# Optimization experiments

Measured on AMD Instinct MI355X. Metric: run time of the kernel, lower is better.

The kernel has to match this reference:

```python
import jax, jax.numpy as jnp
import numpy as np

J = 24
PARENTS = [-1, 0, 0, 0, 1, 2, 3, 4, 5, 6, 7, 8, 9, 9, 9, 12, 13, 14, 16, 17, 18, 19, 20, 21]


def _rodrigues(rvec):
    # rvec: [M,3] axis-angle -> [M,3,3] rotation matrices (Rodrigues formula)
    angle = jnp.linalg.norm(rvec, axis=-1, keepdims=True) + 1e-8  # [M,1]
    axis = rvec / angle
    s = jnp.sin(angle)[..., None]  # [M,1,1]
    c = jnp.cos(angle)[..., None]
    kx, ky, kz = axis[:, 0], axis[:, 1], axis[:, 2]
    zo = jnp.zeros_like(kx)
    K = jnp.stack([zo, -kz, ky, kz, zo, -kx, -ky, kx, zo], axis=-1).reshape(-1, 3, 3)
    eye = jnp.eye(3, dtype=rvec.dtype)
    return eye + s * K + (1.0 - c) * (K @ K)


def _get_tfs(poses, rest_joints, cano_inv=None):
    # poses: [B,J,3] -> relative transforms [B,J,4,4]
    B = poses.shape[0]
    R = _rodrigues(poses.reshape(-1, 3)).reshape(B, J, 3, 3)
    parents = np.asarray(PARENTS)
    rel_j = rest_joints.at[1:].add(-rest_joints[parents[1:]])  # [J,3]
    top = jnp.concatenate([R, jnp.broadcast_to(rel_j[None, :, :, None], (B, J, 3, 1))], axis=-1)
    bot = jnp.broadcast_to(jnp.array([0.0, 0.0, 0.0, 1.0], poses.dtype), (B, J, 1, 4))
    T = jnp.concatenate([top, bot], axis=-2)  # [B,J,4,4]
    chain = [T[:, 0]]
    for i in range(1, J):
        chain.append(chain[parents[i]] @ T[:, i])
    transforms = jnp.stack(chain, axis=1)  # [B,J,4,4]
    # subtract transforms @ [j;0] from the translation column
    tj = jnp.einsum('bjrc,jc->bjr', transforms[..., :3], rest_joints)  # [B,J,4]
    rel = jnp.concatenate([transforms[..., :3], (transforms[..., 3] - tj)[..., None]], axis=-1)
    if cano_inv is not None:
        rel = jnp.einsum('bnij,njk->bnik', rel, cano_inv)
    return rel


def _grid_sample_3d(grid, coords):
    # grid: [C,D,H,W]; coords: [P,3] normalized (x,y,z), align_corners=False, border padding
    C, D, H, W = grid.shape
    sizes = jnp.array([W, H, D], dtype=coords.dtype)
    c = ((coords + 1.0) * sizes - 1.0) * 0.5
    c = jnp.clip(c, 0.0, sizes - 1.0)
    c0f = jnp.floor(c)
    frac = c - c0f  # [P,3]
    c0 = c0f.astype(jnp.int32)
    cmax = (sizes - 1.0).astype(jnp.int32)
    c1 = jnp.minimum(c0 + 1, cmax)
    out = jnp.zeros((C, coords.shape[0]), dtype=grid.dtype)
    for dx in (0, 1):
        for dy in (0, 1):
            for dz in (0, 1):
                ix = c1[:, 0] if dx else c0[:, 0]
                iy = c1[:, 1] if dy else c0[:, 1]
                iz = c1[:, 2] if dz else c0[:, 2]
                wx = frac[:, 0] if dx else 1.0 - frac[:, 0]
                wy = frac[:, 1] if dy else 1.0 - frac[:, 1]
                wz = frac[:, 2] if dz else 1.0 - frac[:, 2]
                out = out + grid[:, iz, iy, ix] * (wx * wy * wz)[None, :]
    return out.T  # [P,C]


def _query_weights(verts, weight_grid, lhand_grid, rhand_grid,
                   bbox_extend, bbox_center, lhand_extend, lhand_center,
                   rhand_extend, rhand_center):
    B, N, _ = verts.shape
    p = ((verts - bbox_center[None, None]) / bbox_extend * 2.0).reshape(B * N, 3)
    w = _grid_sample_3d(weight_grid, p)  # [P,J]
    pl = p * lhand_extend + lhand_center[None]
    lmask = jnp.all((pl >= -1.0) & (pl <= 1.0), axis=-1)
    w = jnp.where(lmask[:, None], _grid_sample_3d(lhand_grid, pl), w)
    pr = p * rhand_extend + rhand_center[None]
    rmask = jnp.all((pr >= -1.0) & (pr <= 1.0), axis=-1)
    w = jnp.where(rmask[:, None], _grid_sample_3d(rhand_grid, pr), w)
    return w.reshape(B, N, J)


def setup_inputs() -> dict:
    key = jax.random.key(0)
    ks = jax.random.split(key, 8)
    B, N, R = 4, 65536, 128
    verts = jax.random.uniform(ks[0], (B, N, 3), jnp.float32, -0.9, 0.9)
    poses = jax.random.normal(ks[1], (B, J, 3), jnp.float32) * 0.2
    cano_pose = jax.random.normal(ks[2], (1, J, 3), jnp.float32) * 0.05
    rest_joints = jax.random.normal(ks[3], (J, 3), jnp.float32) * 0.3
    weight_grid = jax.random.uniform(ks[4], (J, R, R, R), jnp.float32)
    lhand_grid = jax.random.uniform(ks[5], (J, R, R, R), jnp.float32)
    rhand_grid = jax.random.uniform(ks[6], (J, R, R, R), jnp.float32)
    return dict(
        verts=verts, poses=poses, cano_pose=cano_pose, rest_joints=rest_joints,
        weight_grid=weight_grid, lhand_grid=lhand_grid, rhand_grid=rhand_grid,
        bbox_extend=jnp.float32(2.0), bbox_center=jnp.zeros((3,), jnp.float32),
        lhand_extend=jnp.float32(6.0), lhand_center=jnp.array([3.0, 1.2, 0.1], jnp.float32),
        rhand_extend=jnp.float32(6.0), rhand_center=jnp.array([-3.0, 1.2, 0.1], jnp.float32),
    )


def reference(verts, poses, cano_pose, rest_joints, weight_grid, lhand_grid, rhand_grid,
              bbox_extend, bbox_center, lhand_extend, lhand_center, rhand_extend, rhand_center):
    B, N = verts.shape[:2]
    cano_tfs = _get_tfs(cano_pose, rest_joints, None)        # [1,J,4,4]
    cano_inv = jnp.linalg.inv(cano_tfs[0])                   # [J,4,4]
    rel = _get_tfs(poses, rest_joints, cano_inv)             # [B,J,4,4]
    weights = _query_weights(verts, weight_grid, lhand_grid, rhand_grid,
                             bbox_extend, bbox_center, lhand_extend, lhand_center,
                             rhand_extend, rhand_center)     # [B,N,J]
    wt = jnp.matmul(weights, rel.reshape(B, J, 16)).reshape(B, N, 4, 4)
    posed = jnp.einsum('bnij,bnj->bni', wt[..., :3, :3], verts) + wt[..., :3, 3]
    return posed
```

## Files before the change

kernel.cpp:

```cpp
#include <hip/hip_runtime.h>
#include <math.h>

#define J 24
#define RES 128
#define DHW (RES*RES*RES)
#define NBINS 16384

__device__ __constant__ int PARENTS[J] = {-1,0,0,0,1,2,3,4,5,6,7,8,9,9,9,12,13,14,16,17,18,19,20,21};

__device__ inline void compose34(const float* a, const float* b, float* r) {
    for (int i = 0; i < 3; ++i) {
        float a0 = a[i*4+0], a1 = a[i*4+1], a2 = a[i*4+2], a3 = a[i*4+3];
        r[i*4+0] = a0*b[0] + a1*b[4] + a2*b[8];
        r[i*4+1] = a0*b[1] + a1*b[5] + a2*b[9];
        r[i*4+2] = a0*b[2] + a1*b[6] + a2*b[10];
        r[i*4+3] = a0*b[3] + a1*b[7] + a2*b[11] + a3;
    }
}

__global__ void tf_kernel(const float* __restrict__ poses,
                          const float* __restrict__ cano_pose,
                          const float* __restrict__ rest_joints,
                          float* __restrict__ rel_out) {
    __shared__ float M[5][J][12];
    __shared__ float relj[J][3];
    __shared__ float cinv[J][12];
    const int t = threadIdx.x;

    if (t < J) {
        int p = PARENTS[t];
        for (int k = 0; k < 3; ++k) {
            float v = rest_joints[t*3+k];
            if (p >= 0) v -= rest_joints[p*3+k];
            relj[t][k] = v;
        }
    }
    __syncthreads();

    for (int task = t; task < 5*J; task += blockDim.x) {
        int s = task / J, j = task % J;
        const float* rv = (s == 0) ? (cano_pose + j*3) : (poses + ((s-1)*J + j)*3);
        float rx = rv[0], ry = rv[1], rz = rv[2];
        float ang = sqrtf(rx*rx + ry*ry + rz*rz) + 1e-8f;
        float ax = rx/ang, ay = ry/ang, az = rz/ang;
        float s_ = sinf(ang), c_ = cosf(ang), ic = 1.0f - c_;
        float* m = M[s][j];
        m[0]  = 1.0f - ic*(ay*ay + az*az);
        m[1]  = -s_*az + ic*ax*ay;
        m[2]  =  s_*ay + ic*ax*az;
        m[3]  = relj[j][0];
        m[4]  =  s_*az + ic*ax*ay;
        m[5]  = 1.0f - ic*(ax*ax + az*az);
        m[6]  = -s_*ax + ic*ay*az;
        m[7]  = relj[j][1];
        m[8]  = -s_*ay + ic*ax*az;
        m[9]  =  s_*ax + ic*ay*az;
        m[10] = 1.0f - ic*(ax*ax + ay*ay);
        m[11] = relj[j][2];
    }
    __syncthreads();

    if (t < 5) {
        for (int i = 1; i < J; ++i) {
            int p = PARENTS[i];
            float r[12];
            compose34(M[t][p], M[t][i], r);
            for (int k = 0; k < 12; ++k) M[t][i][k] = r[k];
        }
    }
    __syncthreads();

    for (int task = t; task < 5*J; task += blockDim.x) {
        int s = task / J, j = task % J;
        float* m = M[s][j];
        float rjx = rest_joints[j*3], rjy = rest_joints[j*3+1], rjz = rest_joints[j*3+2];
        m[3]  -= m[0]*rjx + m[1]*rjy + m[2]*rjz;
        m[7]  -= m[4]*rjx + m[5]*rjy + m[6]*rjz;
        m[11] -= m[8]*rjx + m[9]*rjy + m[10]*rjz;
    }
    __syncthreads();

    if (t < J) {
        const float* m = M[0][t];
        float* ci = cinv[t];
        ci[0] = m[0]; ci[1] = m[4]; ci[2]  = m[8];
        ci[4] = m[1]; ci[5] = m[5]; ci[6]  = m[9];
        ci[8] = m[2]; ci[9] = m[6]; ci[10] = m[10];
        ci[3]  = -(ci[0]*m[3] + ci[1]*m[7] + ci[2]*m[11]);
        ci[7]  = -(ci[4]*m[3] + ci[5]*m[7] + ci[6]*m[11]);
        ci[11] = -(ci[8]*m[3] + ci[9]*m[7] + ci[10]*m[11]);
    }
    __syncthreads();

    for (int task = t; task < 4*J; task += blockDim.x) {
        int b = task / J, j = task % J;
        float r[12];
        compose34(M[b+1][j], cinv[j], r);
        for (int k = 0; k < 12; ++k) rel_out[(b*J + j)*12 + k] = r[k];
    }
}

__global__ void zero_kernel(unsigned int* __restrict__ p, int n) {
    int i = blockIdx.x * blockDim.x + threadIdx.x;
    if (i < n) p[i] = 0;
}

__device__ inline void main_grid_coords(float vx, float vy, float vz,
                                        float bcx, float bcy, float bcz, float be,
                                        float& px, float& py, float& pz,
                                        int& x0, int& y0, int& z0,
                                        float& tx, float& ty, float& tz) {
    px = (vx - bcx) / be * 2.0f;
    py = (vy - bcy) / be * 2.0f;
    pz = (vz - bcz) / be * 2.0f;
    const float S = (float)RES;
    float fx = ((px + 1.0f) * S - 1.0f) * 0.5f;
    float fy = ((py + 1.0f) * S - 1.0f) * 0.5f;
    float fz = ((pz + 1.0f) * S - 1.0f) * 0.5f;
    fx = fminf(fmaxf(fx, 0.0f), S - 1.0f);
    fy = fminf(fmaxf(fy, 0.0f), S - 1.0f);
    fz = fminf(fmaxf(fz, 0.0f), S - 1.0f);
    float x0f = floorf(fx), y0f = floorf(fy), z0f = floorf(fz);
    tx = fx - x0f; ty = fy - y0f; tz = fz - z0f;
    x0 = (int)x0f; y0 = (int)y0f; z0 = (int)z0f;
}

__global__ __launch_bounds__(256) void key_kernel(
    const float* __restrict__ verts,
    const float* __restrict__ bbox_extend, const float* __restrict__ bbox_center,
    unsigned int* __restrict__ keys, unsigned int* __restrict__ hist, int total) {
    int i = blockIdx.x * blockDim.x + threadIdx.x;
    if (i >= total) return;
    float vx = verts[(size_t)i*3+0], vy = verts[(size_t)i*3+1], vz = verts[(size_t)i*3+2];
    float px, py, pz, tx, ty, tz;
    int x0, y0, z0;
    main_grid_coords(vx, vy, vz, bbox_center[0], bbox_center[1], bbox_center[2],
                     bbox_extend[0], px, py, pz, x0, y0, z0, tx, ty, tz);
    unsigned int key = ((unsigned)z0 << 7) | (unsigned)y0;
    keys[i] = key;
    atomicAdd(&hist[key], 1u);
}

__global__ __launch_bounds__(1024) void scan_kernel(
    const unsigned int* __restrict__ hist, unsigned int* __restrict__ cursor) {
    __shared__ unsigned int partial[1024];
    const int t = threadIdx.x;
    const int CHUNK = NBINS / 1024;
    unsigned int local[CHUNK];
    unsigned int s = 0;
    #pragma unroll
    for (int k = 0; k < CHUNK; ++k) { local[k] = s; s += hist[t*CHUNK + k]; }
    partial[t] = s;
    __syncthreads();
    for (int off = 1; off < 1024; off <<= 1) {
        unsigned int v = (t >= off) ? partial[t - off] : 0u;
        __syncthreads();
        partial[t] += v;
        __syncthreads();
    }
    unsigned int excl = partial[t] - s;
    #pragma unroll
    for (int k = 0; k < CHUNK; ++k) cursor[t*CHUNK + k] = excl + local[k];
}

__global__ __launch_bounds__(256) void scatter_kernel(
    const unsigned int* __restrict__ keys, unsigned int* __restrict__ cursor,
    unsigned int* __restrict__ order, int total) {
    int i = blockIdx.x * blockDim.x + threadIdx.x;
    if (i >= total) return;
    unsigned int key = keys[i];
    unsigned int pos = atomicAdd(&cursor[key], 1u);
    order[pos] = (unsigned int)i;
}

__device__ inline void sample_grid_f32(const float* __restrict__ g,
                                       float cx, float cy, float cz, float* w) {
    const float S = (float)RES;
    float fx = ((cx + 1.0f) * S - 1.0f) * 0.5f;
    float fy = ((cy + 1.0f) * S - 1.0f) * 0.5f;
    float fz = ((cz + 1.0f) * S - 1.0f) * 0.5f;
    fx = fminf(fmaxf(fx, 0.0f), S - 1.0f);
    fy = fminf(fmaxf(fy, 0.0f), S - 1.0f);
    fz = fminf(fmaxf(fz, 0.0f), S - 1.0f);
    float x0f = floorf(fx), y0f = floorf(fy), z0f = floorf(fz);
    float tx = fx - x0f, ty = fy - y0f, tz = fz - z0f;
    int x0 = (int)x0f, y0 = (int)y0f, z0 = (int)z0f;
    int x1 = x0 < RES-1 ? x0+1 : RES-1;
    int y1 = y0 < RES-1 ? y0+1 : RES-1;
    int z1 = z0 < RES-1 ? z0+1 : RES-1;
    int b00 = (z0*RES + y0)*RES;
    int b01 = (z0*RES + y1)*RES;
    int b10 = (z1*RES + y0)*RES;
    int b11 = (z1*RES + y1)*RES;
    float wx0 = 1.0f - tx, wx1 = tx;
    float wy0 = 1.0f - ty, wy1 = ty;
    float wz0 = 1.0f - tz, wz1 = tz;
    float w000 = wz0*wy0*wx0, w001 = wz0*wy0*wx1;
    float w010 = wz0*wy1*wx0, w011 = wz0*wy1*wx1;
    float w100 = wz1*wy0*wx0, w101 = wz1*wy0*wx1;
    float w110 = wz1*wy1*wx0, w111 = wz1*wy1*wx1;
    #pragma unroll
    for (int c = 0; c < J; ++c) {
        const float* gc = g + (size_t)c * DHW;
        w[c] = gc[b00+x0]*w000 + gc[b00+x1]*w001
             + gc[b01+x0]*w010 + gc[b01+x1]*w011
             + gc[b10+x0]*w100 + gc[b10+x1]*w101
             + gc[b11+x0]*w110 + gc[b11+x1]*w111;
    }
}

__global__ __launch_bounds__(256) void skin_sorted(
    const float* __restrict__ verts,
    const float* __restrict__ wgrid,
    const float* __restrict__ lgrid,
    const float* __restrict__ rgrid,
    const float* __restrict__ rel,
    const unsigned int* __restrict__ order,
    const float* __restrict__ bbox_extend, const float* __restrict__ bbox_center,
    const float* __restrict__ lhand_extend, const float* __restrict__ lhand_center,
    const float* __restrict__ rhand_extend, const float* __restrict__ rhand_center,
    float* __restrict__ out, int N, int total) {
    __shared__ float srel[4*J*12];
    for (int i = threadIdx.x; i < 4*J*12; i += blockDim.x)
        srel[i] = rel[i];
    __syncthreads();

    int sid = blockIdx.x * blockDim.x + threadIdx.x;
    if (sid >= total) return;
    int pid = (int)order[sid];
    int b = pid / N;

    float vx = verts[(size_t)pid*3 + 0];
    float vy = verts[(size_t)pid*3 + 1];
    float vz = verts[(size_t)pid*3 + 2];

    float px, py, pz, tx, ty, tz;
    int x0, y0, z0;
    main_grid_coords(vx, vy, vz, bbox_center[0], bbox_center[1], bbox_center[2],
                     bbox_extend[0], px, py, pz, x0, y0, z0, tx, ty, tz);
    int x1 = x0 < RES-1 ? x0+1 : RES-1;
    int y1 = y0 < RES-1 ? y0+1 : RES-1;
    int z1 = z0 < RES-1 ? z0+1 : RES-1;
    int b00 = (z0*RES + y0)*RES;
    int b01 = (z0*RES + y1)*RES;
    int b10 = (z1*RES + y0)*RES;
    int b11 = (z1*RES + y1)*RES;
    float wx0 = 1.0f - tx, wx1 = tx;
    float wy0 = 1.0f - ty, wy1 = ty;
    float wz0 = 1.0f - tz, wz1 = tz;
    float w000 = wz0*wy0*wx0, w001 = wz0*wy0*wx1;
    float w010 = wz0*wy1*wx0, w011 = wz0*wy1*wx1;
    float w100 = wz1*wy0*wx0, w101 = wz1*wy0*wx1;
    float w110 = wz1*wy1*wx0, w111 = wz1*wy1*wx1;

    float w[J];
    #pragma unroll
    for (int c = 0; c < J; ++c) {
        const float* gc = wgrid + (size_t)c * DHW;
        w[c] = gc[b00+x0]*w000 + gc[b00+x1]*w001
             + gc[b01+x0]*w010 + gc[b01+x1]*w011
             + gc[b10+x0]*w100 + gc[b10+x1]*w101
             + gc[b11+x0]*w110 + gc[b11+x1]*w111;
    }

    float le = lhand_extend[0];
    float plx = px*le + lhand_center[0];
    float ply = py*le + lhand_center[1];
    float plz = pz*le + lhand_center[2];
    if (plx >= -1.0f && plx <= 1.0f && ply >= -1.0f && ply <= 1.0f &&
        plz >= -1.0f && plz <= 1.0f) {
        sample_grid_f32(lgrid, plx, ply, plz, w);
    }
    float re = rhand_extend[0];
    float prx = px*re + rhand_center[0];
    float pry = py*re + rhand_center[1];
    float prz = pz*re + rhand_center[2];
    if (prx >= -1.0f && prx <= 1.0f && pry >= -1.0f && pry <= 1.0f &&
        prz >= -1.0f && prz <= 1.0f) {
        sample_grid_f32(rgrid, prx, pry, prz, w);
    }

    const float* rb = &srel[b*J*12];
    float m[12];
    #pragma unroll
    for (int k = 0; k < 12; ++k) m[k] = 0.0f;
    #pragma unroll
    for (int j = 0; j < J; ++j) {
        float wj = w[j];
        const float* rj = &rb[j*12];
        #pragma unroll
        for (int k = 0; k < 12; ++k) m[k] += wj * rj[k];
    }

    out[(size_t)pid*3 + 0] = m[0]*vx + m[1]*vy + m[2]*vz  + m[3];
    out[(size_t)pid*3 + 1] = m[4]*vx + m[5]*vy + m[6]*vz  + m[7];
    out[(size_t)pid*3 + 2] = m[8]*vx + m[9]*vy + m[10]*vz + m[11];
}

extern "C" void kernel_launch(void* const* d_in, const int* in_sizes, int n_in,
                              void* d_out, int out_size, void* d_ws, size_t ws_size,
                              hipStream_t stream) {
    const float* verts       = (const float*)d_in[0];
    const float* poses       = (const float*)d_in[1];
    const float* cano_pose   = (const float*)d_in[2];
    const float* rest_joints = (const float*)d_in[3];
    const float* wgrid       = (const float*)d_in[4];
    const float* lgrid       = (const float*)d_in[5];
    const float* rgrid       = (const float*)d_in[6];
    const float* bbox_extend = (const float*)d_in[7];
    const float* bbox_center = (const float*)d_in[8];
    const float* lhand_extend= (const float*)d_in[9];
    const float* lhand_center= (const float*)d_in[10];
    const float* rhand_extend= (const float*)d_in[11];
    const float* rhand_center= (const float*)d_in[12];

    float* out = (float*)d_out;

    const int B = 4;
    const int total = in_sizes[0] / 3;
    const int N = total / B;

    char* ws = (char*)d_ws;
    float*        rel    = (float*)(ws);
    unsigned int* hist   = (unsigned int*)(ws + 8192);
    unsigned int* cursor = (unsigned int*)(ws + 8192 + 65536);
    unsigned int* keys   = (unsigned int*)(ws + 8192 + 2*65536);
    unsigned int* order  = (unsigned int*)(ws + 8192 + 2*65536 + (size_t)total*4);

    const int block = 256;
    const int pgrid = (total + block - 1) / block;

    tf_kernel<<<1, 128, 0, stream>>>(poses, cano_pose, rest_joints, rel);
    zero_kernel<<<(NBINS + block - 1) / block, block, 0, stream>>>(hist, NBINS);
    key_kernel<<<pgrid, block, 0, stream>>>(verts, bbox_extend, bbox_center,
                                            keys, hist, total);
    scan_kernel<<<1, 1024, 0, stream>>>(hist, cursor);
    scatter_kernel<<<pgrid, block, 0, stream>>>(keys, cursor, order, total);
    skin_sorted<<<pgrid, block, 0, stream>>>(
        verts, wgrid, lgrid, rgrid, rel, order,
        bbox_extend, bbox_center, lhand_extend, lhand_center,
        rhand_extend, rhand_center, out, N, total);
}
```

Measured before the change: 126.4 us.

## Split joints across thread pairs, paired x loads, finer sort keys

Each point is now handled by two threads, each sampling 12 of the 24 weight channels. The partial blended transforms are combined with a shuffle. Grid reads fetch adjacent x voxels as one 8-byte load, and the rel table is transposed in shared memory so each batch index is interleaved. The sort key now includes coarse x bits, giving 16x more histogram bins and a reworked scan, to improve locality. Costs: the per-point coordinate work is duplicated, the key and scan stages grow, and the 8-byte loads may be unaligned.

```diff
diff --git a/kernel.cpp b/kernel.cpp
--- a/kernel.cpp
+++ b/kernel.cpp
@@ -4,9 +4,13 @@
 #define J 24
 #define RES 128
 #define DHW (RES*RES*RES)
-#define NBINS 16384
+#define NBINS (128*128*16)
 
 __device__ __constant__ int PARENTS[J] = {-1,0,0,0,1,2,3,4,5,6,7,8,9,9,9,12,13,14,16,17,18,19,20,21};
+
+struct __attribute__((packed, aligned(4))) f2u {
+    float x, y;
+};
 
 __device__ inline void compose34(const float* a, const float* b, float* r) {
     for (int i = 0; i < 3; ++i) {
@@ -136,7 +140,7 @@
     int x0, y0, z0;
     main_grid_coords(vx, vy, vz, bbox_center[0], bbox_center[1], bbox_center[2],
                      bbox_extend[0], px, py, pz, x0, y0, z0, tx, ty, tz);
-    unsigned int key = ((unsigned)z0 << 7) | (unsigned)y0;
+    unsigned int key = ((unsigned)z0 << 11) | ((unsigned)y0 << 4) | ((unsigned)x0 >> 3);
     keys[i] = key;
     atomicAdd(&hist[key], 1u);
 }
@@ -146,10 +150,9 @@
     __shared__ unsigned int partial[1024];
     const int t = threadIdx.x;
     const int CHUNK = NBINS / 1024;
-    unsigned int local[CHUNK];
+    const int base = t * CHUNK;
     unsigned int s = 0;
-    #pragma unroll
-    for (int k = 0; k < CHUNK; ++k) { local[k] = s; s += hist[t*CHUNK + k]; }
+    for (int k = 0; k < CHUNK; ++k) s += hist[base + k];
     partial[t] = s;
     __syncthreads();
     for (int off = 1; off < 1024; off <<= 1) {
@@ -158,9 +161,11 @@
         partial[t] += v;
         __syncthreads();
     }
-    unsigned int excl = partial[t] - s;
-    #pragma unroll
-    for (int k = 0; k < CHUNK; ++k) cursor[t*CHUNK + k] = excl + local[k];
+    unsigned int run = partial[t] - s;
+    for (int k = 0; k < CHUNK; ++k) {
+        cursor[base + k] = run;
+        run += hist[base + k];
+    }
 }
 
 __global__ __launch_bounds__(256) void scatter_kernel(
@@ -173,8 +178,8 @@
     order[pos] = (unsigned int)i;
 }
 
-__device__ inline void sample_grid_f32(const float* __restrict__ g,
-                                       float cx, float cy, float cz, float* w) {
+__device__ inline void sample_hand12(const float* __restrict__ g, int c0,
+                                     float cx, float cy, float cz, float* w12) {
     const float S = (float)RES;
     float fx = ((cx + 1.0f) * S - 1.0f) * 0.5f;
     float fy = ((cy + 1.0f) * S - 1.0f) * 0.5f;
@@ -200,12 +205,12 @@
     float w100 = wz1*wy0*wx0, w101 = wz1*wy0*wx1;
     float w110 = wz1*wy1*wx0, w111 = wz1*wy1*wx1;
     #pragma unroll
-    for (int c = 0; c < J; ++c) {
-        const float* gc = g + (size_t)c * DHW;
-        w[c] = gc[b00+x0]*w000 + gc[b00+x1]*w001
-             + gc[b01+x0]*w010 + gc[b01+x1]*w011
-             + gc[b10+x0]*w100 + gc[b10+x1]*w101
-             + gc[b11+x0]*w110 + gc[b11+x1]*w111;
+    for (int c = 0; c < 12; ++c) {
+        const float* gc = g + (size_t)(c0 + c) * DHW;
+        w12[c] = gc[b00+x0]*w000 + gc[b00+x1]*w001
+               + gc[b01+x0]*w010 + gc[b01+x1]*w011
+               + gc[b10+x0]*w100 + gc[b10+x1]*w101
+               + gc[b11+x0]*w110 + gc[b11+x1]*w111;
     }
 }
 
@@ -220,12 +225,16 @@
     const float* __restrict__ lhand_extend, const float* __restrict__ lhand_center,
     const float* __restrict__ rhand_extend, const float* __restrict__ rhand_center,
     float* __restrict__ out, int N, int total) {
-    __shared__ float srel[4*J*12];
-    for (int i = threadIdx.x; i < 4*J*12; i += blockDim.x)
-        srel[i] = rel[i];
-    __syncthreads();
-
-    int sid = blockIdx.x * blockDim.x + threadIdx.x;
+    __shared__ float srel_t[J*12*4];
+    for (int i = threadIdx.x; i < 4*J*12; i += blockDim.x) {
+        int b = i & 3, jk = i >> 2;
+        srel_t[i] = rel[b*J*12 + jk];
+    }
+    __syncthreads();
+
+    int gid = blockIdx.x * blockDim.x + threadIdx.x;
+    int sid = gid >> 1;
+    int half = gid & 1;
     if (sid >= total) return;
     int pid = (int)order[sid];
     int b = pid / N;
@@ -238,7 +247,6 @@
     int x0, y0, z0;
     main_grid_coords(vx, vy, vz, bbox_center[0], bbox_center[1], bbox_center[2],
                      bbox_extend[0], px, py, pz, x0, y0, z0, tx, ty, tz);
-    int x1 = x0 < RES-1 ? x0+1 : RES-1;
     int y1 = y0 < RES-1 ? y0+1 : RES-1;
     int z1 = z0 < RES-1 ? z0+1 : RES-1;
     int b00 = (z0*RES + y0)*RES;
@@ -248,19 +256,28 @@
     float wx0 = 1.0f - tx, wx1 = tx;
     float wy0 = 1.0f - ty, wy1 = ty;
     float wz0 = 1.0f - tz, wz1 = tz;
-    float w000 = wz0*wy0*wx0, w001 = wz0*wy0*wx1;
-    float w010 = wz0*wy1*wx0, w011 = wz0*wy1*wx1;
-    float w100 = wz1*wy0*wx0, w101 = wz1*wy0*wx1;
-    float w110 = wz1*wy1*wx0, w111 = wz1*wy1*wx1;
-
-    float w[J];
-    #pragma unroll
-    for (int c = 0; c < J; ++c) {
-        const float* gc = wgrid + (size_t)c * DHW;
-        w[c] = gc[b00+x0]*w000 + gc[b00+x1]*w001
-             + gc[b01+x0]*w010 + gc[b01+x1]*w011
-             + gc[b10+x0]*w100 + gc[b10+x1]*w101
-             + gc[b11+x0]*w110 + gc[b11+x1]*w111;
+    float r00 = wz0*wy0, r01 = wz0*wy1, r10 = wz1*wy0, r11 = wz1*wy1;
+
+    int xb = x0 < 127 ? x0 : 126;
+    bool hi = (x0 == 127);
+    const int c0 = half * 12;
+
+    float w[12];
+    #pragma unroll
+    for (int c = 0; c < 12; ++c) {
+        const float* gc = wgrid + (size_t)(c0 + c) * DHW;
+        f2u v00 = *(const f2u*)(gc + b00 + xb);
+        f2u v01 = *(const f2u*)(gc + b01 + xb);
+        f2u v10 = *(const f2u*)(gc + b10 + xb);
+        f2u v11 = *(const f2u*)(gc + b11 + xb);
+        float a00 = hi ? v00.y : v00.x;
+        float a01 = hi ? v01.y : v01.x;
+        float a10 = hi ? v10.y : v10.x;
+        float a11 = hi ? v11.y : v11.x;
+        w[c] = r00 * (wx0*a00 + wx1*v00.y)
+             + r01 * (wx0*a01 + wx1*v01.y)
+             + r10 * (wx0*a10 + wx1*v10.y)
+             + r11 * (wx0*a11 + wx1*v11.y);
     }
 
     float le = lhand_extend[0];
@@ -269,7 +286,7 @@
     float plz = pz*le + lhand_center[2];
     if (plx >= -1.0f && plx <= 1.0f && ply >= -1.0f && ply <= 1.0f &&
         plz >= -1.0f && plz <= 1.0f) {
-        sample_grid_f32(lgrid, plx, ply, plz, w);
+        sample_hand12(lgrid, c0, plx, ply, plz, w);
     }
     float re = rhand_extend[0];
     float prx = px*re + rhand_center[0];
@@ -277,24 +294,27 @@
     float prz = pz*re + rhand_center[2];
     if (prx >= -1.0f && prx <= 1.0f && pry >= -1.0f && pry <= 1.0f &&
         prz >= -1.0f && prz <= 1.0f) {
-        sample_grid_f32(rgrid, prx, pry, prz, w);
-    }
-
-    const float* rb = &srel[b*J*12];
+        sample_hand12(rgrid, c0, prx, pry, prz, w);
+    }
+
     float m[12];
     #pragma unroll
     for (int k = 0; k < 12; ++k) m[k] = 0.0f;
     #pragma unroll
-    for (int j = 0; j < J; ++j) {
-        float wj = w[j];
-        const float* rj = &rb[j*12];
+    for (int c = 0; c < 12; ++c) {
+        float wj = w[c];
+        const float* rj = &srel_t[((c0 + c)*12)*4 + b];
         #pragma unroll
-        for (int k = 0; k < 12; ++k) m[k] += wj * rj[k];
-    }
-
-    out[(size_t)pid*3 + 0] = m[0]*vx + m[1]*vy + m[2]*vz  + m[3];
-    out[(size_t)pid*3 + 1] = m[4]*vx + m[5]*vy + m[6]*vz  + m[7];
-    out[(size_t)pid*3 + 2] = m[8]*vx + m[9]*vy + m[10]*vz + m[11];
+        for (int k = 0; k < 12; ++k) m[k] += wj * rj[k*4];
+    }
+    #pragma unroll
+    for (int k = 0; k < 12; ++k) m[k] += __shfl_xor(m[k], 1);
+
+    if (half == 0) {
+        out[(size_t)pid*3 + 0] = m[0]*vx + m[1]*vy + m[2]*vz  + m[3];
+        out[(size_t)pid*3 + 1] = m[4]*vx + m[5]*vy + m[6]*vz  + m[7];
+        out[(size_t)pid*3 + 2] = m[8]*vx + m[9]*vy + m[10]*vz + m[11];
+    }
 }
 
 extern "C" void kernel_launch(void* const* d_in, const int* in_sizes, int n_in,
@@ -323,9 +343,9 @@
     char* ws = (char*)d_ws;
     float*        rel    = (float*)(ws);
     unsigned int* hist   = (unsigned int*)(ws + 8192);
-    unsigned int* cursor = (unsigned int*)(ws + 8192 + 65536);
-    unsigned int* keys   = (unsigned int*)(ws + 8192 + 2*65536);
-    unsigned int* order  = (unsigned int*)(ws + 8192 + 2*65536 + (size_t)total*4);
+    unsigned int* cursor = (unsigned int*)(ws + 8192 + NBINS*4);
+    unsigned int* keys   = (unsigned int*)(ws + 8192 + 2*(size_t)NBINS*4);
+    unsigned int* order  = (unsigned int*)(ws + 8192 + 2*(size_t)NBINS*4 + (size_t)total*4);
 
     const int block = 256;
     const int pgrid = (total + block - 1) / block;
@@ -336,7 +356,9 @@
                                             keys, hist, total);
     scan_kernel<<<1, 1024, 0, stream>>>(hist, cursor);
     scatter_kernel<<<pgrid, block, 0, stream>>>(keys, cursor, order, total);
-    skin_sorted<<<pgrid, block, 0, stream>>>(
+
+    const int sgrid = (total*2 + block - 1) / block;
+    skin_sorted<<<sgrid, block, 0, stream>>>(
         verts, wgrid, lgrid, rgrid, rel, order,
         bbox_extend, bbox_center, lhand_extend, lhand_center,
         rhand_extend, rhand_center, out, N, total);
```

Result: slower. 219.0 us (+73.2%).
